# Performance work log

Measured on AMD Instinct MI355X. Metric: run time of the kernel, lower is better.

Reference implementation:

```python
import jax, jax.numpy as jnp
import numpy as np

TEMP = 0.05
ALPHA = 0.1
EPS = 1e-12


def setup_inputs() -> dict:
    key = jax.random.key(0)
    k1, k2, k3, k4 = jax.random.split(key, 4)
    bs, emb_dim, n_class, n_aux = 16384, 512, 2000, 5
    features = jax.random.normal(k1, (bs, emb_dim), dtype=jnp.float32)
    word_embed = jax.random.normal(k2, (n_class, emb_dim), dtype=jnp.float32)
    label = jax.random.randint(k3, (bs,), 0, n_class)
    aux = jax.random.randint(k4, (bs, n_aux), 0, n_class)
    return {"features": features, "word_embed": word_embed, "label": label, "aux": aux}


def _cosine_logits(features, word_embed):
    # F.normalize(x, dim=-1): x / max(||x||, eps)
    f = features / jnp.maximum(jnp.linalg.norm(features, axis=-1, keepdims=True), EPS)
    w = word_embed / jnp.maximum(jnp.linalg.norm(word_embed, axis=-1, keepdims=True), EPS)
    return jnp.matmul(f, w.T) / TEMP  # (bs, n_class)


def reference(features, word_embed, label, aux):
    pred = _cosine_logits(features, word_embed)
    lse = jax.nn.logsumexp(pred, axis=1)                                  # log sum exp per row
    tgt = jnp.take_along_axis(pred, label[:, None], axis=1)[:, 0]         # pred[i, target[i]]
    # normal cross entropy: mean_i(-pred[i,t_i] + log sum exp(pred[i]))
    loss_normal = jnp.mean(-tgt + lse)
    # label-smoothing CE: -(1-a)*pred[i,t_i] + lse - (a/n_aux)*sum_j pred[i, aux[i,j]]
    single_alpha = ALPHA / aux.shape[-1]
    aux_logits = jnp.take_along_axis(pred, aux, axis=1)                   # (bs, n_aux)
    loss_ls = jnp.mean(-(1.0 - ALPHA) * tgt + lse - single_alpha * jnp.sum(aux_logits, axis=1))
    loss = 0.5 * (loss_normal + loss_ls)
    acc = jnp.mean((jnp.argmax(pred, axis=1) == label).astype(jnp.float32))
    return loss, acc
```

## Files before the change

### kernel.cpp

```cpp
#include <hip/hip_runtime.h>
#include <hip/hip_bf16.h>
#include <hip/hip_fp8.h>
#include <stdint.h>

#define BS   16384
#define NC   2000
#define NCP  2048
#define EMB  512
#define NAUX 5
#define NCHUNK 32
#define GBLK 4096

typedef __bf16 bf16x8 __attribute__((ext_vector_type(8)));
typedef float  f32x4  __attribute__((ext_vector_type(4)));

__global__ __launch_bounds__(256) void norm_kernel(
    const float* __restrict__ feat, const float* __restrict__ wemb,
    unsigned char* __restrict__ fn8, unsigned char* __restrict__ wn8,
    __bf16* __restrict__ fnb, __bf16* __restrict__ wnb)
{
    const int lane = threadIdx.x & 63;
    const int wv   = threadIdx.x >> 6;
    const int row  = blockIdx.x * 4 + wv;

    if (row >= BS + NC) {
        const int pr = row - BS;
        *(unsigned*)(wn8 + (size_t)pr * EMB + lane * 4)       = 0u;
        *(unsigned*)(wn8 + (size_t)pr * EMB + 256 + lane * 4) = 0u;
        ushort4 z = {0, 0, 0, 0};
        ((ushort4*)(wnb + (size_t)pr * EMB))[lane]      = z;
        ((ushort4*)(wnb + (size_t)pr * EMB))[64 + lane] = z;
        return;
    }
    const float* src;
    unsigned char* dst8;
    __bf16* dstb;
    if (row < BS) { src = feat + (size_t)row * EMB;
                    dst8 = fn8 + (size_t)row * EMB;        dstb = fnb + (size_t)row * EMB; }
    else          { src = wemb + (size_t)(row - BS) * EMB;
                    dst8 = wn8 + (size_t)(row - BS) * EMB; dstb = wnb + (size_t)(row - BS) * EMB; }

    const float4* s4 = (const float4*)src;
    float4 x = s4[lane];
    float4 y = s4[64 + lane];

    float ss = x.x * x.x + x.y * x.y + x.z * x.z + x.w * x.w
             + y.x * y.x + y.y * y.y + y.z * y.z + y.w * y.w;
    #pragma unroll
    for (int m = 1; m < 64; m <<= 1) ss += __shfl_xor(ss, m, 64);
    const float scale = 1.0f / fmaxf(sqrtf(ss), 1e-12f);

    float v[8];
    v[0] = x.x * scale; v[1] = x.y * scale; v[2] = x.z * scale; v[3] = x.w * scale;
    v[4] = y.x * scale; v[5] = y.y * scale; v[6] = y.z * scale; v[7] = y.w * scale;

    __bf16 b[8];
    #pragma unroll
    for (int j = 0; j < 8; ++j) b[j] = (__bf16)v[j];
    *(ushort4*)(dstb + 4 * lane)       = *(const ushort4*)(b);
    *(ushort4*)(dstb + 256 + 4 * lane) = *(const ushort4*)(b + 4);

    int p0 = 0, p1 = 0;
    p0 = __builtin_amdgcn_cvt_pk_fp8_f32(v[0], v[1], p0, false);
    p0 = __builtin_amdgcn_cvt_pk_fp8_f32(v[2], v[3], p0, true);
    p1 = __builtin_amdgcn_cvt_pk_fp8_f32(v[4], v[5], p1, false);
    p1 = __builtin_amdgcn_cvt_pk_fp8_f32(v[6], v[7], p1, true);
    *(int*)(dst8 + 4 * lane)       = p0;
    *(int*)(dst8 + 256 + 4 * lane) = p1;
}

__global__ __launch_bounds__(256) void main_kernel(
    const unsigned char* __restrict__ fn8, const unsigned char* __restrict__ wn8,
    float* __restrict__ es_p, unsigned* __restrict__ key_p)
{
    __shared__ __align__(16) unsigned char As[128 * 128];
    __shared__ __align__(16) unsigned char Bs[128 * 128];

    const int tid   = threadIdx.x;
    const int lane  = tid & 63;
    const int l15   = lane & 15;
    const int quad  = lane >> 4;
    const int wv    = tid >> 6;
    const int wvM   = wv >> 1;
    const int wvN   = wv & 1;
    const int xcd   = blockIdx.x & 7;
    const int j     = blockIdx.x >> 3;
    const int mTile = xcd * 16 + (j >> 4);
    const int nTile = j & 15;

    const unsigned char* fbase = fn8 + (size_t)mTile * 128 * EMB;
    const unsigned char* wbase = wn8 + (size_t)nTile * 128 * EMB;

    const int rIn8 = lane >> 3;
    const int cLog = (lane & 7) ^ rIn8;

    f32x4 acc[4][4] = {};

    #pragma unroll
    for (int t = 0; t < 4; ++t) {
        __syncthreads();
        #pragma unroll
        for (int p = 0; p < 4; ++p) {
            const int slot = wv * 4 + p;
            const int row  = slot * 8 + rIn8;
            const size_t goff = (size_t)row * EMB + (size_t)t * 128 + (size_t)cLog * 16;
            __builtin_amdgcn_global_load_lds(
                (const __attribute__((address_space(1))) void*)(fbase + goff),
                (__attribute__((address_space(3))) void*)(As + slot * 1024), 16, 0, 0);
            __builtin_amdgcn_global_load_lds(
                (const __attribute__((address_space(1))) void*)(wbase + goff),
                (__attribute__((address_space(3))) void*)(Bs + slot * 1024), 16, 0, 0);
        }
        __builtin_amdgcn_s_waitcnt(0);
        __syncthreads();

        #pragma unroll
        for (int kc = 0; kc < 4; ++kc) {
            long aF[4], bF[4];
            const int c16  = kc * 2 + (quad >> 1);
            const int hoff = (quad & 1) << 3;
            #pragma unroll
            for (int i = 0; i < 4; ++i) {
                const int ar = wvM * 64 + i * 16 + l15;
                const int br = wvN * 64 + i * 16 + l15;
                const int ca = ((c16 ^ (l15 & 7)) << 4) + hoff;
                aF[i] = *(const long*)(As + ar * 128 + ca);
                bF[i] = *(const long*)(Bs + br * 128 + ca);
            }
            #pragma unroll
            for (int mi = 0; mi < 4; ++mi)
                #pragma unroll
                for (int ni = 0; ni < 4; ++ni)
                    acc[mi][ni] = __builtin_amdgcn_mfma_f32_16x16x32_fp8_fp8(
                        aF[mi], bF[ni], acc[mi][ni], 0, 0, 0);
        }
    }

    const float C20 = 28.853900817779268f;
    const int chunk = nTile * 2 + wvN;
    #pragma unroll
    for (int mi = 0; mi < 4; ++mi) {
        float    es[4] = {0.f, 0.f, 0.f, 0.f};
        unsigned km[4] = {0u, 0u, 0u, 0u};
        #pragma unroll
        for (int ni = 0; ni < 4; ++ni) {
            const int col = nTile * 128 + wvN * 64 + ni * 16 + l15;
            const unsigned colenc = 2047u - (unsigned)col;
            const bool valid = (col < NC);
            #pragma unroll
            for (int r = 0; r < 4; ++r) {
                float v = valid ? acc[mi][ni][r] : -3.0f;
                es[r] += exp2f((v - 1.0f) * C20);
                unsigned u = __float_as_uint(v);
                unsigned k = u ^ (unsigned)(((int)u >> 31) | 0x80000000);
                unsigned pk = (k & 0xFFFFF800u) | colenc;
                km[r] = pk > km[r] ? pk : km[r];
            }
        }
        #pragma unroll
        for (int r = 0; r < 4; ++r) {
            #pragma unroll
            for (int m = 1; m < 16; m <<= 1) {
                es[r] += __shfl_xor(es[r], m, 64);
                unsigned x = __shfl_xor(km[r], m, 64);
                km[r] = x > km[r] ? x : km[r];
            }
        }
        if (l15 == 0) {
            #pragma unroll
            for (int r = 0; r < 4; ++r) {
                const int row = mTile * 128 + wvM * 64 + mi * 16 + quad * 4 + r;
                es_p [(size_t)row * NCHUNK + chunk] = es[r];
                key_p[(size_t)row * NCHUNK + chunk] = km[r];
            }
        }
    }
}

__global__ __launch_bounds__(256) void gather_fin_kernel(
    const __bf16* __restrict__ fnb, const __bf16* __restrict__ wnb,
    const int* __restrict__ label, const int* __restrict__ aux,
    const float* __restrict__ es_p, const unsigned* __restrict__ key_p,
    float* __restrict__ blkpart)
{
    const int lane = threadIdx.x & 63;
    const int wv   = threadIdx.x >> 6;
    const int row  = blockIdx.x * 4 + wv;

    const int cch = lane & 31;
    float    es = es_p [(size_t)row * NCHUNK + cch];
    unsigned k  = key_p[(size_t)row * NCHUNK + cch];

    const int lab = label[row];
    int cols[6];
    cols[0] = lab;
    #pragma unroll
    for (int j = 0; j < NAUX; ++j) cols[j + 1] = aux[row * NAUX + j];

    bf16x8 f8 = *((const bf16x8*)fnb + (size_t)row * (EMB / 8) + lane);

    bf16x8 w8[6];
    #pragma unroll
    for (int c = 0; c < 6; ++c)
        w8[c] = *((const bf16x8*)wnb + (size_t)cols[c] * (EMB / 8) + lane);

    float fv[8];
    #pragma unroll
    for (int j = 0; j < 8; ++j) fv[j] = (float)f8[j];

    float d[6];
    #pragma unroll
    for (int c = 0; c < 6; ++c) {
        float t = 0.f;
        #pragma unroll
        for (int j = 0; j < 8; ++j) t += fv[j] * (float)w8[c][j];
        d[c] = t;
    }

    #pragma unroll
    for (int m = 1; m < 64; m <<= 1) {
        #pragma unroll
        for (int c = 0; c < 6; ++c) d[c] += __shfl_xor(d[c], m, 64);
        if (m < 32) {
            es += __shfl_xor(es, m, 64);
            unsigned x = __shfl_xor(k, m, 64);
            k = x > k ? x : k;
        }
    }

    const float tgt  = d[0] * 20.0f;
    const float auxs = (d[1] + d[2] + d[3] + d[4] + d[5]) * 20.0f;
    const int amax = 2047 - (int)(k & 0x7FFu);
    const float loss = 20.0f + logf(es) - 0.95f * tgt - 0.01f * auxs;
    const float acc  = (amax == lab) ? 1.0f : 0.0f;

    __shared__ float sl[4], sa[4];
    if (lane == 0) { sl[wv] = loss; sa[wv] = acc; }
    __syncthreads();
    if (threadIdx.x == 0) {
        blkpart[blockIdx.x]        = sl[0] + sl[1] + sl[2] + sl[3];
        blkpart[GBLK + blockIdx.x] = sa[0] + sa[1] + sa[2] + sa[3];
    }
}

__global__ __launch_bounds__(256) void fin2_kernel(
    const float* __restrict__ blkpart, float* __restrict__ out)
{
    float l = 0.f, a = 0.f;
    #pragma unroll
    for (int i = 0; i < GBLK / 256; ++i) {
        l += blkpart[i * 256 + threadIdx.x];
        a += blkpart[GBLK + i * 256 + threadIdx.x];
    }
    #pragma unroll
    for (int m = 1; m < 64; m <<= 1) {
        l += __shfl_xor(l, m, 64);
        a += __shfl_xor(a, m, 64);
    }
    __shared__ float sl[4], sa[4];
    const int wv = threadIdx.x >> 6;
    if ((threadIdx.x & 63) == 0) { sl[wv] = l; sa[wv] = a; }
    __syncthreads();
    if (threadIdx.x == 0) {
        out[0] = (sl[0] + sl[1] + sl[2] + sl[3]) / (float)BS;
        out[1] = (sa[0] + sa[1] + sa[2] + sa[3]) / (float)BS;
    }
}

extern "C" void kernel_launch(void* const* d_in, const int* in_sizes, int n_in,
                              void* d_out, int out_size, void* d_ws, size_t ws_size,
                              hipStream_t stream)
{
    const float* feat  = (const float*)d_in[0];
    const float* wemb  = (const float*)d_in[1];
    const int*   label = (const int*)d_in[2];
    const int*   aux   = (const int*)d_in[3];

    char* ws = (char*)d_ws;
    unsigned char* fn8     = (unsigned char*)(ws);
    unsigned char* wn8     = (unsigned char*)(ws + 8388608);
    __bf16*        fnb     = (__bf16*)(ws + 9437184);
    __bf16*        wnb     = (__bf16*)(ws + 26214400);
    float*         es_p    = (float*)(ws + 28311552);
    unsigned*      key_p   = (unsigned*)(ws + 30408704);
    float*         blkpart = (float*)(ws + 32505856);
    float*         out     = (float*)d_out;

    hipLaunchKernelGGL(norm_kernel, dim3((BS + NCP) / 4), dim3(256), 0, stream,
                       feat, wemb, fn8, wn8, fnb, wnb);
    hipLaunchKernelGGL(main_kernel, dim3((BS / 128) * (NCP / 128)), dim3(256), 0, stream,
                       fn8, wn8, es_p, key_p);
    hipLaunchKernelGGL(gather_fin_kernel, dim3(GBLK), dim3(256), 0, stream,
                       fnb, wnb, label, aux, es_p, key_p, blkpart);
    hipLaunchKernelGGL(fin2_kernel, dim3(1), dim3(256), 0, stream, blkpart, out);
}
```

Measured before the change: 132.6 us.

## Double-buffer LDS staging with smaller K tiles to overlap loads and MFMA

The GEMM main loop goes from four K-steps of 128 bytes, each with a full wait, to eight K-steps of 64 bytes over two LDS buffers. The next tiles are prefetched with async global-to-LDS loads while MFMAs run on the current buffer, using vmcnt-based partial waits. The LDS swizzle is reworked to pack two rows per 128-byte line. This hides global load latency behind compute at the cost of more barriers, and the hand-tuned waitcnt values must match the number of loads in flight.

After: 133.5 us. No clear change (+0.7%).

```diff
diff --git a/kernel.cpp b/kernel.cpp
--- a/kernel.cpp
+++ b/kernel.cpp
@@ -73,8 +73,8 @@
     const unsigned char* __restrict__ fn8, const unsigned char* __restrict__ wn8,
     float* __restrict__ es_p, unsigned* __restrict__ key_p)
 {
-    __shared__ __align__(16) unsigned char As[128 * 128];
-    __shared__ __align__(16) unsigned char Bs[128 * 128];
+    __shared__ __align__(16) unsigned char As[2][8192];
+    __shared__ __align__(16) unsigned char Bs[2][8192];
 
     const int tid   = threadIdx.x;
     const int lane  = tid & 63;
@@ -91,31 +91,40 @@
     const unsigned char* fbase = fn8 + (size_t)mTile * 128 * EMB;
     const unsigned char* wbase = wn8 + (size_t)nTile * 128 * EMB;
 
-    const int rIn8 = lane >> 3;
-    const int cLog = (lane & 7) ^ rIn8;
+    const int r8   = lane >> 3;
+    const int chv  = (lane & 7) ^ r8;
+    const int gc16 = chv & 3;
+    const int rowB = r8 * 2 + (chv >> 2);
 
     f32x4 acc[4][4] = {};
 
-    #pragma unroll
-    for (int t = 0; t < 4; ++t) {
-        __syncthreads();
-        #pragma unroll
-        for (int p = 0; p < 4; ++p) {
-            const int slot = wv * 4 + p;
-            const int row  = slot * 8 + rIn8;
-            const size_t goff = (size_t)row * EMB + (size_t)t * 128 + (size_t)cLog * 16;
+    auto STAGE = [&](int t, int buf) {
+        #pragma unroll
+        for (int p = 0; p < 2; ++p) {
+            const int slot = wv * 2 + p;
+            const int grow = slot * 16 + rowB;
+            const size_t goff = (size_t)grow * EMB + (size_t)t * 64 + (size_t)gc16 * 16;
             __builtin_amdgcn_global_load_lds(
                 (const __attribute__((address_space(1))) void*)(fbase + goff),
-                (__attribute__((address_space(3))) void*)(As + slot * 1024), 16, 0, 0);
+                (__attribute__((address_space(3))) void*)(&As[buf][slot * 1024]), 16, 0, 0);
             __builtin_amdgcn_global_load_lds(
                 (const __attribute__((address_space(1))) void*)(wbase + goff),
-                (__attribute__((address_space(3))) void*)(Bs + slot * 1024), 16, 0, 0);
-        }
-        __builtin_amdgcn_s_waitcnt(0);
-        __syncthreads();
-
-        #pragma unroll
-        for (int kc = 0; kc < 4; ++kc) {
+                (__attribute__((address_space(3))) void*)(&Bs[buf][slot * 1024]), 16, 0, 0);
+        }
+    };
+
+    STAGE(0, 0);
+    STAGE(1, 1);
+
+    #pragma unroll
+    for (int t = 0; t < 8; ++t) {
+        if (t < 7) asm volatile("s_waitcnt vmcnt(4)" ::: "memory");
+        else       asm volatile("s_waitcnt vmcnt(0)" ::: "memory");
+        __builtin_amdgcn_s_barrier();
+
+        const int cur = t & 1;
+        #pragma unroll
+        for (int kc = 0; kc < 2; ++kc) {
             long aF[4], bF[4];
             const int c16  = kc * 2 + (quad >> 1);
             const int hoff = (quad & 1) << 3;
@@ -123,9 +132,10 @@
             for (int i = 0; i < 4; ++i) {
                 const int ar = wvM * 64 + i * 16 + l15;
                 const int br = wvN * 64 + i * 16 + l15;
-                const int ca = ((c16 ^ (l15 & 7)) << 4) + hoff;
-                aF[i] = *(const long*)(As + ar * 128 + ca);
-                bF[i] = *(const long*)(Bs + br * 128 + ca);
+                const int pa = ((((ar & 1) << 2) + c16) ^ ((ar >> 1) & 7)) * 16 + hoff;
+                const int pb = ((((br & 1) << 2) + c16) ^ ((br >> 1) & 7)) * 16 + hoff;
+                aF[i] = *(const long*)(&As[cur][(ar >> 1) * 128 + pa]);
+                bF[i] = *(const long*)(&Bs[cur][(br >> 1) * 128 + pb]);
             }
             #pragma unroll
             for (int mi = 0; mi < 4; ++mi)
@@ -133,6 +143,12 @@
                 for (int ni = 0; ni < 4; ++ni)
                     acc[mi][ni] = __builtin_amdgcn_mfma_f32_16x16x32_fp8_fp8(
                         aF[mi], bF[ni], acc[mi][ni], 0, 0, 0);
+        }
+
+        if (t < 6) {
+            asm volatile("s_waitcnt lgkmcnt(0)" ::: "memory");
+            __builtin_amdgcn_s_barrier();
+            STAGE(t + 2, cur);
         }
     }
 
```
